# Kernel optimization log

Measured on AMD Instinct MI355X. Metric: run time of the kernel, lower is better.

Reference implementation:

```python
import jax, jax.numpy as jnp
import numpy as np

B, L, C, H = 32, 2048, 1280, 160  # batch, seq, channels=1280 (hard-coded), hidden=1280//8


def setup_inputs() -> dict:
    key = jax.random.key(0)
    k1, k2, k3 = jax.random.split(key, 3)
    x = jax.random.normal(k1, (B, L, C), dtype=jnp.float32)
    w1 = jax.random.normal(k2, (C, H), dtype=jnp.float32) * 0.02
    b1 = jnp.zeros((H,), dtype=jnp.float32)
    w2 = jax.random.normal(k3, (H, C), dtype=jnp.float32) * 0.02
    b2 = jnp.zeros((C,), dtype=jnp.float32)
    return {"x": x, "w1": w1, "b1": b1, "w2": w2, "b2": b2}


def _mlp(v, w1, b1, w2, b2):
    # shared 2-layer MLP: Dense(C->H, relu) -> Dense(H->C)
    h = jax.nn.relu(v @ w1 + b1)
    return h @ w2 + b2


def reference(x, w1, b1, w2, b2):
    gap = jnp.mean(x, axis=1)  # [B, C] global average pool over seq
    gmp = jnp.max(x, axis=1)   # [B, C] global max pool over seq
    attn = jax.nn.sigmoid(_mlp(gap, w1, b1, w2, b2) + _mlp(gmp, w1, b1, w2, b2))  # [B, C]
    return x * attn[:, None, :]  # channel-wise gate broadcast over seq
```

## Files before the change

kernel.cpp:

```cpp
#include <hip/hip_runtime.h>
#include <hip/hip_fp16.h>
#include <math.h>

#define BB 32
#define LL 2048
#define CC 1280
#define HH 160
#define LCH 32
#define LCHP 32
#define PPB 16

typedef float    f4 __attribute__((ext_vector_type(4)));
typedef float    f8 __attribute__((ext_vector_type(8)));
typedef _Float16 h8 __attribute__((ext_vector_type(8)));


__global__ __launch_bounds__(320) void pool_conv_k(
    const float* __restrict__ x, float* __restrict__ psum,
    float* __restrict__ pmax, _Float16* __restrict__ xh) {
  const int lcb = blockIdx.x;
  const int b   = blockIdx.y;
  const int t   = threadIdx.x;
  const int c4  = t << 2;

  const int lp0 = lcb * 32;
  const float* xp = x + ((size_t)b * LL + (size_t)lp0 * 2) * CC + c4;
  _Float16*    hp = xh + ((size_t)b * (LL / 2) + lp0) * (2 * CC) + (size_t)t * 8;

  f4 s = {0.f, 0.f, 0.f, 0.f};
  f4 m = {-INFINITY, -INFINITY, -INFINITY, -INFINITY};

#pragma unroll 8
  for (int p = 0; p < 32; ++p) {
    const float* row = xp + (size_t)p * (2 * CC);
    f4 v0 = __builtin_nontemporal_load(reinterpret_cast<const f4*>(row));
    f4 v1 = __builtin_nontemporal_load(reinterpret_cast<const f4*>(row + CC));
    s += v0;
    s += v1;
    m.x = fmaxf(m.x, fmaxf(v0.x, v1.x));
    m.y = fmaxf(m.y, fmaxf(v0.y, v1.y));
    m.z = fmaxf(m.z, fmaxf(v0.z, v1.z));
    m.w = fmaxf(m.w, fmaxf(v0.w, v1.w));
    f8 w = __builtin_shufflevector(v0, v1, 0, 1, 2, 3, 4, 5, 6, 7);
    *reinterpret_cast<h8*>(hp + (size_t)p * (2 * CC)) = __builtin_convertvector(w, h8);
  }
  const size_t o = ((size_t)lcb * BB + b) * CC + c4;
  *reinterpret_cast<f4*>(psum + o) = s;
  *reinterpret_cast<f4*>(pmax + o) = m;
}

__global__ __launch_bounds__(320) void pool_k(
    const float* __restrict__ x, float* __restrict__ psum,
    float* __restrict__ pmax) {
  const int lcb = blockIdx.x;
  const int b   = blockIdx.y;
  const int c4  = threadIdx.x << 2;

  const float* xp = x + ((size_t)b * LL + (size_t)lcb * 64) * CC + c4;
  f4 s = {0.f, 0.f, 0.f, 0.f};
  f4 m = {-INFINITY, -INFINITY, -INFINITY, -INFINITY};
#pragma unroll 8
  for (int l = 0; l < 64; ++l) {
    f4 v = *reinterpret_cast<const f4*>(xp + (size_t)l * CC);
    s += v;
    m.x = fmaxf(m.x, v.x); m.y = fmaxf(m.y, v.y);
    m.z = fmaxf(m.z, v.z); m.w = fmaxf(m.w, v.w);
  }
  const size_t o = ((size_t)lcb * BB + b) * CC + c4;
  *reinterpret_cast<f4*>(psum + o) = s;
  *reinterpret_cast<f4*>(pmax + o) = m;
}

__global__ __launch_bounds__(320) void finish_l1_k(
    const float* __restrict__ psum, const float* __restrict__ pmax,
    const float* __restrict__ w1, const float* __restrict__ b1,
    float* __restrict__ hout) {
  __shared__ float v[CC];
  __shared__ float part[HH];

  const int r = blockIdx.x;
  const int t = threadIdx.x;
  const int b = r & (BB - 1);
  const bool ismax = (r >= BB);

  for (int c = t; c < CC; c += 320) {
    if (!ismax) {
      float s = 0.f;
      for (int lc = 0; lc < LCHP; ++lc)
        s += psum[((size_t)lc * BB + b) * CC + c];
      v[c] = s * (1.0f / (float)LL);
    } else {
      float m = -INFINITY;
      for (int lc = 0; lc < LCHP; ++lc)
        m = fmaxf(m, pmax[((size_t)lc * BB + b) * CC + c]);
      v[c] = m;
    }
  }
  __syncthreads();

  const int h  = (t < HH) ? t : t - HH;
  const int k0 = (t < HH) ? 0 : CC / 2;
  float acc = 0.f;
#pragma unroll 8
  for (int k = 0; k < CC / 2; ++k)
    acc = fmaf(v[k0 + k], w1[(size_t)(k0 + k) * HH + h], acc);
  if (t >= HH) part[h] = acc;
  __syncthreads();
  if (t < HH) {
    float a = acc + part[t] + b1[t];
    hout[(size_t)r * HH + t] = fmaxf(a, 0.f);
  }
}

__global__ __launch_bounds__(256) void layer2_k(
    const float* __restrict__ hout, const float* __restrict__ w2,
    const float* __restrict__ b2, float* __restrict__ attn) {
  __shared__ float u[HH];
  const int b  = blockIdx.y;
  const int ct = blockIdx.x;
  const int t  = threadIdx.x;

  if (t < HH)
    u[t] = hout[(size_t)b * HH + t] + hout[(size_t)(b + BB) * HH + t];
  __syncthreads();

  const int c = ct * 256 + t;
  float acc = 2.0f * b2[c];
#pragma unroll 8
  for (int h = 0; h < HH; ++h)
    acc = fmaf(u[h], w2[(size_t)h * CC + c], acc);
  attn[(size_t)b * CC + c] = 1.0f / (1.0f + expf(-acc));
}

__global__ __launch_bounds__(320) void apply_h_k(
    const _Float16* __restrict__ xh, const float* __restrict__ attn,
    float* __restrict__ out) {
  const int t  = threadIdx.x;
  const int c4 = t << 2;
  const size_t pg0 = (size_t)(gridDim.x - 1 - blockIdx.x) * PPB;
  const int b = (int)(pg0 >> 10);
  const int lp = (int)(pg0 & 1023);

  const f4 a = *reinterpret_cast<const f4*>(attn + (size_t)b * CC + c4);
  const _Float16* hp = xh + pg0 * (2 * CC) + (size_t)t * 8;
  float* op = out + ((size_t)b * LL + (size_t)lp * 2) * CC + c4;

#pragma unroll
  for (int i = 0; i < PPB; ++i) {
    h8 hv = *reinterpret_cast<const h8*>(hp + (size_t)i * (2 * CC));
    f8 v = __builtin_convertvector(hv, f8);
    f4 v0 = __builtin_shufflevector(v, v, 0, 1, 2, 3);
    f4 v1 = __builtin_shufflevector(v, v, 4, 5, 6, 7);
    f4 o0 = v0 * a;
    f4 o1 = v1 * a;
    float* orow = op + (size_t)i * (2 * CC);
    __builtin_nontemporal_store(o0, reinterpret_cast<f4*>(orow));
    __builtin_nontemporal_store(o1, reinterpret_cast<f4*>(orow + CC));
  }
}

__global__ __launch_bounds__(320) void apply_f_k(
    const float* __restrict__ x, const float* __restrict__ attn,
    float* __restrict__ out) {
  const size_t r0 = (size_t)(gridDim.x - 1 - blockIdx.x) * 8;
  const int b = (int)(r0 >> 11);
  const int c4 = threadIdx.x << 2;

  const f4 a = *reinterpret_cast<const f4*>(attn + (size_t)b * CC + c4);
  const float* xp = x + r0 * CC + c4;
  float* op = out + r0 * CC + c4;

#pragma unroll
  for (int i = 0; i < 8; ++i) {
    f4 v = *reinterpret_cast<const f4*>(xp + (size_t)i * CC);
    f4 o = v * a;
    __builtin_nontemporal_store(o, reinterpret_cast<f4*>(op + (size_t)i * CC));
  }
}

extern "C" void kernel_launch(void* const* d_in, const int* in_sizes, int n_in,
                              void* d_out, int out_size, void* d_ws, size_t ws_size,
                              hipStream_t stream) {
  const float* x  = (const float*)d_in[0];
  const float* w1 = (const float*)d_in[1];
  const float* b1 = (const float*)d_in[2];
  const float* w2 = (const float*)d_in[3];
  const float* b2 = (const float*)d_in[4];
  float* out = (float*)d_out;

  const size_t n_x = (size_t)BB * LL * CC;
  const size_t f32_elems = (size_t)LCHP * BB * CC * 2 + (size_t)2 * BB * HH + (size_t)BB * CC;
  const bool use_h = ws_size >= n_x * sizeof(_Float16) + f32_elems * sizeof(float);

  _Float16* xh = (_Float16*)d_ws;
  float* fbase = use_h ? (float*)((char*)d_ws + n_x * sizeof(_Float16)) : (float*)d_ws;
  float* psum = fbase;
  float* pmax = psum + (size_t)LCHP * BB * CC;
  float* hout = pmax + (size_t)LCHP * BB * CC;
  float* attn = hout + (size_t)2 * BB * HH;

  if (use_h)
    pool_conv_k<<<dim3(LCH, BB), 320, 0, stream>>>(x, psum, pmax, xh);
  else
    pool_k<<<dim3(LCH, BB), 320, 0, stream>>>(x, psum, pmax);

  finish_l1_k<<<2 * BB, 320, 0, stream>>>(psum, pmax, w1, b1, hout);
  layer2_k<<<dim3(CC / 256, BB), 256, 0, stream>>>(hout, w2, b2, attn);

  if (use_h)
    apply_h_k<<<BB * LL / 2 / PPB, 320, 0, stream>>>(xh, attn, out);
  else
    apply_f_k<<<BB * LL / 8, 320, 0, stream>>>(x, attn, out);
}
```

Measured before the change: 223.5 us.

## Fuse MLP kernels into one and switch fp16 cache to natural row layout

Merges the two MLP kernels into a single per-batch kernel that reduces the pooled partials, runs both dense layers and the sigmoid, which removes one launch and the intermediate hidden buffer. The fp16 copy of x now uses the plain row-major layout: the pooling kernel does one row per iteration with half4 stores instead of paired-row half8 stores, and the apply kernel reads half8 per thread across 8 channels. The fused MLP uses only 32 blocks, with each thread running the full 1280-length dot product, so it may run longer than the split version. Plain loads replace the nontemporal loads in the pooling pass.

```diff
diff --git a/kernel.cpp b/kernel.cpp
--- a/kernel.cpp
+++ b/kernel.cpp
@@ -8,45 +8,116 @@
 #define HH 160
 #define LCH 32
 #define LCHP 32
-#define PPB 16
 
 typedef float    f4 __attribute__((ext_vector_type(4)));
 typedef float    f8 __attribute__((ext_vector_type(8)));
+typedef _Float16 h4 __attribute__((ext_vector_type(4)));
 typedef _Float16 h8 __attribute__((ext_vector_type(8)));
-
 
 __global__ __launch_bounds__(320) void pool_conv_k(
     const float* __restrict__ x, float* __restrict__ psum,
     float* __restrict__ pmax, _Float16* __restrict__ xh) {
   const int lcb = blockIdx.x;
   const int b   = blockIdx.y;
-  const int t   = threadIdx.x;
-  const int c4  = t << 2;
+  const int c4  = threadIdx.x << 2;
 
-  const int lp0 = lcb * 32;
-  const float* xp = x + ((size_t)b * LL + (size_t)lp0 * 2) * CC + c4;
-  _Float16*    hp = xh + ((size_t)b * (LL / 2) + lp0) * (2 * CC) + (size_t)t * 8;
+  const size_t row0 = (size_t)b * LL + (size_t)lcb * 64;
+  const float* xp = x  + row0 * CC + c4;
+  _Float16*    hp = xh + row0 * CC + c4;
 
   f4 s = {0.f, 0.f, 0.f, 0.f};
   f4 m = {-INFINITY, -INFINITY, -INFINITY, -INFINITY};
 
 #pragma unroll 8
-  for (int p = 0; p < 32; ++p) {
-    const float* row = xp + (size_t)p * (2 * CC);
-    f4 v0 = __builtin_nontemporal_load(reinterpret_cast<const f4*>(row));
-    f4 v1 = __builtin_nontemporal_load(reinterpret_cast<const f4*>(row + CC));
-    s += v0;
-    s += v1;
-    m.x = fmaxf(m.x, fmaxf(v0.x, v1.x));
-    m.y = fmaxf(m.y, fmaxf(v0.y, v1.y));
-    m.z = fmaxf(m.z, fmaxf(v0.z, v1.z));
-    m.w = fmaxf(m.w, fmaxf(v0.w, v1.w));
-    f8 w = __builtin_shufflevector(v0, v1, 0, 1, 2, 3, 4, 5, 6, 7);
-    *reinterpret_cast<h8*>(hp + (size_t)p * (2 * CC)) = __builtin_convertvector(w, h8);
+  for (int l = 0; l < 64; ++l) {
+    f4 v = *reinterpret_cast<const f4*>(xp + (size_t)l * CC);
+    s += v;
+    m.x = fmaxf(m.x, v.x); m.y = fmaxf(m.y, v.y);
+    m.z = fmaxf(m.z, v.z); m.w = fmaxf(m.w, v.w);
+    *reinterpret_cast<h4*>(hp + (size_t)l * CC) = __builtin_convertvector(v, h4);
   }
   const size_t o = ((size_t)lcb * BB + b) * CC + c4;
   *reinterpret_cast<f4*>(psum + o) = s;
   *reinterpret_cast<f4*>(pmax + o) = m;
+}
+
+__global__ __launch_bounds__(320) void mlp_k(
+    const float* __restrict__ psum, const float* __restrict__ pmax,
+    const float* __restrict__ w1, const float* __restrict__ b1,
+    const float* __restrict__ w2, const float* __restrict__ b2,
+    float* __restrict__ attn) {
+  __shared__ float vg[CC];
+  __shared__ float vm[CC];
+  __shared__ float h1[HH];
+  __shared__ float h2[HH];
+
+  const int b = blockIdx.x;
+  const int t = threadIdx.x;
+
+  for (int c = t; c < CC; c += 320) {
+    float s = 0.f, mm = -INFINITY;
+    for (int lc = 0; lc < LCHP; ++lc) {
+      const size_t o = ((size_t)lc * BB + b) * CC + c;
+      s += psum[o];
+      mm = fmaxf(mm, pmax[o]);
+    }
+    vg[c] = s * (1.0f / (float)LL);
+    vm[c] = mm;
+  }
+  __syncthreads();
+
+  {
+    const float* v = (t < HH) ? vg : vm;
+    const int h = (t < HH) ? t : t - HH;
+    float acc = b1[h];
+#pragma unroll 8
+    for (int k = 0; k < CC; ++k)
+      acc = fmaf(v[k], w1[(size_t)k * HH + h], acc);
+    acc = fmaxf(acc, 0.f);
+    if (t < HH) h1[h] = acc; else h2[h] = acc;
+  }
+  __syncthreads();
+
+  for (int c = t; c < CC; c += 320) {
+    float acc = 2.0f * b2[c];
+#pragma unroll 8
+    for (int h = 0; h < HH; ++h)
+      acc = fmaf(h1[h] + h2[h], w2[(size_t)h * CC + c], acc);
+    attn[(size_t)b * CC + c] = 1.0f / (1.0f + expf(-acc));
+  }
+}
+
+__global__ __launch_bounds__(320) void apply_h_k(
+    const _Float16* __restrict__ xh, const float* __restrict__ attn,
+    float* __restrict__ out) {
+  const size_t blk = (size_t)(gridDim.x - 1 - blockIdx.x);
+  const size_t r0  = blk * 16;
+  const int b = (int)(r0 >> 11);
+  const int t = threadIdx.x;
+  const int half = (t >= 160) ? 1 : 0;
+  const int lane = t - half * 160;
+  const int c8 = lane << 3;
+
+  const float* ap = attn + (size_t)b * CC + c8;
+  const f4 a0 = *reinterpret_cast<const f4*>(ap);
+  const f4 a1 = *reinterpret_cast<const f4*>(ap + 4);
+
+  const size_t base = (r0 + half) * CC + c8;
+  const _Float16* hp = xh + base;
+  float* op = out + base;
+
+#pragma unroll
+  for (int i = 0; i < 8; ++i) {
+    const size_t off = (size_t)i * (2 * CC);
+    h8 hv = *reinterpret_cast<const h8*>(hp + off);
+    f8 v = __builtin_convertvector(hv, f8);
+    f4 v0 = __builtin_shufflevector(v, v, 0, 1, 2, 3);
+    f4 v1 = __builtin_shufflevector(v, v, 4, 5, 6, 7);
+    f4 o0 = v0 * a0;
+    f4 o1 = v1 * a1;
+    __builtin_nontemporal_store(o0, reinterpret_cast<f4*>(op + off));
+    __builtin_nontemporal_store(o1, reinterpret_cast<f4*>(op + off + 4));
+  }
 }
 
 __global__ __launch_bounds__(320) void pool_k(
@@ -69,94 +140,6 @@
   const size_t o = ((size_t)lcb * BB + b) * CC + c4;
   *reinterpret_cast<f4*>(psum + o) = s;
   *reinterpret_cast<f4*>(pmax + o) = m;
-}
-
-__global__ __launch_bounds__(320) void finish_l1_k(
-    const float* __restrict__ psum, const float* __restrict__ pmax,
-    const float* __restrict__ w1, const float* __restrict__ b1,
-    float* __restrict__ hout) {
-  __shared__ float v[CC];
-  __shared__ float part[HH];
-
-  const int r = blockIdx.x;
-  const int t = threadIdx.x;
-  const int b = r & (BB - 1);
-  const bool ismax = (r >= BB);
-
-  for (int c = t; c < CC; c += 320) {
-    if (!ismax) {
-      float s = 0.f;
-      for (int lc = 0; lc < LCHP; ++lc)
-        s += psum[((size_t)lc * BB + b) * CC + c];
-      v[c] = s * (1.0f / (float)LL);
-    } else {
-      float m = -INFINITY;
-      for (int lc = 0; lc < LCHP; ++lc)
-        m = fmaxf(m, pmax[((size_t)lc * BB + b) * CC + c]);
-      v[c] = m;
-    }
-  }
-  __syncthreads();
-
-  const int h  = (t < HH) ? t : t - HH;
-  const int k0 = (t < HH) ? 0 : CC / 2;
-  float acc = 0.f;
-#pragma unroll 8
-  for (int k = 0; k < CC / 2; ++k)
-    acc = fmaf(v[k0 + k], w1[(size_t)(k0 + k) * HH + h], acc);
-  if (t >= HH) part[h] = acc;
-  __syncthreads();
-  if (t < HH) {
-    float a = acc + part[t] + b1[t];
-    hout[(size_t)r * HH + t] = fmaxf(a, 0.f);
-  }
-}
-
-__global__ __launch_bounds__(256) void layer2_k(
-    const float* __restrict__ hout, const float* __restrict__ w2,
-    const float* __restrict__ b2, float* __restrict__ attn) {
-  __shared__ float u[HH];
-  const int b  = blockIdx.y;
-  const int ct = blockIdx.x;
-  const int t  = threadIdx.x;
-
-  if (t < HH)
-    u[t] = hout[(size_t)b * HH + t] + hout[(size_t)(b + BB) * HH + t];
-  __syncthreads();
-
-  const int c = ct * 256 + t;
-  float acc = 2.0f * b2[c];
-#pragma unroll 8
-  for (int h = 0; h < HH; ++h)
-    acc = fmaf(u[h], w2[(size_t)h * CC + c], acc);
-  attn[(size_t)b * CC + c] = 1.0f / (1.0f + expf(-acc));
-}
-
-__global__ __launch_bounds__(320) void apply_h_k(
-    const _Float16* __restrict__ xh, const float* __restrict__ attn,
-    float* __restrict__ out) {
-  const int t  = threadIdx.x;
-  const int c4 = t << 2;
-  const size_t pg0 = (size_t)(gridDim.x - 1 - blockIdx.x) * PPB;
-  const int b = (int)(pg0 >> 10);
-  const int lp = (int)(pg0 & 1023);
-
-  const f4 a = *reinterpret_cast<const f4*>(attn + (size_t)b * CC + c4);
-  const _Float16* hp = xh + pg0 * (2 * CC) + (size_t)t * 8;
-  float* op = out + ((size_t)b * LL + (size_t)lp * 2) * CC + c4;
-
-#pragma unroll
-  for (int i = 0; i < PPB; ++i) {
-    h8 hv = *reinterpret_cast<const h8*>(hp + (size_t)i * (2 * CC));
-    f8 v = __builtin_convertvector(hv, f8);
-    f4 v0 = __builtin_shufflevector(v, v, 0, 1, 2, 3);
-    f4 v1 = __builtin_shufflevector(v, v, 4, 5, 6, 7);
-    f4 o0 = v0 * a;
-    f4 o1 = v1 * a;
-    float* orow = op + (size_t)i * (2 * CC);
-    __builtin_nontemporal_store(o0, reinterpret_cast<f4*>(orow));
-    __builtin_nontemporal_store(o1, reinterpret_cast<f4*>(orow + CC));
-  }
 }
 
 __global__ __launch_bounds__(320) void apply_f_k(
@@ -189,26 +172,24 @@
   float* out = (float*)d_out;
 
   const size_t n_x = (size_t)BB * LL * CC;
-  const size_t f32_elems = (size_t)LCHP * BB * CC * 2 + (size_t)2 * BB * HH + (size_t)BB * CC;
+  const size_t f32_elems = (size_t)LCHP * BB * CC * 2 + (size_t)BB * CC;
   const bool use_h = ws_size >= n_x * sizeof(_Float16) + f32_elems * sizeof(float);
 
   _Float16* xh = (_Float16*)d_ws;
   float* fbase = use_h ? (float*)((char*)d_ws + n_x * sizeof(_Float16)) : (float*)d_ws;
   float* psum = fbase;
   float* pmax = psum + (size_t)LCHP * BB * CC;
-  float* hout = pmax + (size_t)LCHP * BB * CC;
-  float* attn = hout + (size_t)2 * BB * HH;
+  float* attn = pmax + (size_t)LCHP * BB * CC;
 
   if (use_h)
     pool_conv_k<<<dim3(LCH, BB), 320, 0, stream>>>(x, psum, pmax, xh);
   else
     pool_k<<<dim3(LCH, BB), 320, 0, stream>>>(x, psum, pmax);
 
-  finish_l1_k<<<2 * BB, 320, 0, stream>>>(psum, pmax, w1, b1, hout);
-  layer2_k<<<dim3(CC / 256, BB), 256, 0, stream>>>(hout, w2, b2, attn);
+  mlp_k<<<BB, 320, 0, stream>>>(psum, pmax, w1, b1, w2, b2, attn);
 
   if (use_h)
-    apply_h_k<<<BB * LL / 2 / PPB, 320, 0, stream>>>(xh, attn, out);
+    apply_h_k<<<BB * LL / 16, 320, 0, stream>>>(xh, attn, out);
   else
     apply_f_k<<<BB * LL / 8, 320, 0, stream>>>(x, attn, out);
 }
```

Result: slower. 337.0 us (+50.8%).
